# Performance work log

Hardware: AMD Instinct MI355X
Metric: run time of the kernel (lower is better)

The kernel has to match this reference:

```python
import jax, jax.numpy as jnp
import numpy as np

B, D, C = 32, 30, 4        # batch, input spatial, in-channels
KS = 3                     # kernel size per dim
OD = D - KS + 1            # 28 (valid padding, stride 1)
P = OD ** 3                # 21952 output positions
K = (KS ** 3) * C          # 108 taps per output position
F = 4                      # output filters


def _patches(x):
    # x: [B, D, D, D, C] -> [B, P, K]
    xt = jnp.transpose(x, (0, 4, 1, 2, 3))  # NCDHW
    p = jax.lax.conv_general_dilated_patches(
        xt, filter_shape=(KS, KS, KS), window_strides=(1, 1, 1), padding='VALID')
    # p: [B, C*KS^3, OD, OD, OD]
    p = jnp.transpose(p, (0, 2, 3, 4, 1))
    return p.reshape(p.shape[0], P, K)


def _local_conv(x, W):
    # Locally-connected 3D conv (unshared weights) == structured sparse matmul.
    # W: [P, K, F] one weight per (output position, tap, filter).
    return jnp.einsum('bpk,pkf->bpf', _patches(x), W)


def setup_inputs() -> dict:
    key = jax.random.key(0)
    ks = jax.random.split(key, 7)
    x = jax.random.normal(ks[0], (B, D, D, D, C), jnp.float32)
    kernel_loc = jax.random.normal(ks[1], (P, K, F), jnp.float32) * 0.05
    kernel_rho = jax.random.normal(ks[2], (P, K, F), jnp.float32) * 0.1 - 5.0  # softplus -> small scale
    bias = jax.random.normal(ks[3], (F,), jnp.float32) * 0.05
    eps = jax.random.normal(ks[4], (P, K, F), jnp.float32)
    sign_in = jax.random.rademacher(ks[5], (B, D, D, D, C), jnp.float32)
    sign_out = jax.random.rademacher(ks[6], (B, P, F), jnp.float32)
    return dict(x=x, kernel_loc=kernel_loc, kernel_rho=kernel_rho, bias=bias,
                eps=eps, sign_in=sign_in, sign_out=sign_out)


def reference(x, kernel_loc, kernel_rho, bias, eps, sign_in, sign_out):
    # Flipout estimator: deterministic mean path + sign-perturbed noise path.
    scale = jax.nn.softplus(kernel_rho)
    out = _local_conv(x, kernel_loc)                                  # [B, P, F]
    out = out + sign_out * _local_conv(x * sign_in, scale * eps)      # flipout perturbation
    out = out + bias                                                  # per-filter bias (channels_last)
    return out.reshape(x.shape[0], OD, OD, OD, F)
```

## Files before the change

kernel.cpp:

```cpp
#include <hip/hip_runtime.h>


constexpr int Bn   = 32;
constexpr int Dn   = 30;
constexpr int Cn   = 4;
constexpr int ODn  = 28;
constexpr int Pn   = ODn * ODn * ODn;
constexpr int Tt   = 27;
constexpr int Kn   = Tt * Cn;
constexpr int PPB  = 16;
constexpr int THREADS = 256;
constexpr int WSTRIDE = Kn + 1;

__device__ __forceinline__ unsigned bf16rne(float f) {
    unsigned u = __float_as_uint(f);
    return (u + 0x7fffu + ((u >> 16) & 1u)) >> 16;
}
__device__ __forceinline__ float bflo(unsigned u) { return __uint_as_float(u << 16); }
__device__ __forceinline__ float bfhi(unsigned u) { return __uint_as_float(u & 0xffff0000u); }

__global__ __launch_bounds__(THREADS) void lc3d_flipout_kernel(
    const float* __restrict__ x,
    const float* __restrict__ loc,
    const float* __restrict__ rho,
    const float* __restrict__ bias,
    const float* __restrict__ eps,
    const float* __restrict__ sgn_in,
    const float* __restrict__ sgn_out,
    float* __restrict__ out)
{
    __shared__ uint4 w[PPB * WSTRIDE];

    const int tid    = threadIdx.x;
    const int p_base = blockIdx.x * PPB;

    const float4* loc4 = (const float4*)loc + (size_t)p_base * Kn;
    const float4* rho4 = (const float4*)rho + (size_t)p_base * Kn;
    const float4* eps4 = (const float4*)eps + (size_t)p_base * Kn;

    for (int g = tid; g < PPB * Kn; g += THREADS) {
        const int pl = g / Kn;
        const int k  = g - pl * Kn;
        const float4 L = loc4[g];
        const float4 R = rho4[g];
        const float4 E = eps4[g];
        float nx = (R.x > 15.f ? R.x : __logf(1.f + __expf(R.x))) * E.x;
        float ny = (R.y > 15.f ? R.y : __logf(1.f + __expf(R.y))) * E.y;
        float nz = (R.z > 15.f ? R.z : __logf(1.f + __expf(R.z))) * E.z;
        float nw = (R.w > 15.f ? R.w : __logf(1.f + __expf(R.w))) * E.w;
        uint4 pk;
        pk.x = bf16rne(L.x) | (bf16rne(L.y) << 16);
        pk.y = bf16rne(L.z) | (bf16rne(L.w) << 16);
        pk.z = bf16rne(nx)  | (bf16rne(ny) << 16);
        pk.w = bf16rne(nz)  | (bf16rne(nw) << 16);
        w[pl * WSTRIDE + k] = pk;
    }
    __syncthreads();

    const int pl = tid & 15;
    const int bh = tid >> 4;
    const int b0 = bh, b1 = bh + 16;
    const int p  = p_base + pl;
    const int od   = p / (ODn * ODn);
    const int prem = p - od * (ODn * ODn);
    const int oh   = prem / ODn;
    const int ow   = prem - oh * ODn;

    const float4* x4 = (const float4*)x;
    const float4* s4 = (const float4*)sgn_in;
    const size_t v0 = (((size_t)b0 * Dn + od) * Dn + oh) * Dn + ow;
    const size_t v1 = (((size_t)b1 * Dn + od) * Dn + oh) * Dn + ow;
    const uint4* wp = w + pl * WSTRIDE;

    float a00=0.f,a01=0.f,a02=0.f,a03=0.f;
    float a10=0.f,a11=0.f,a12=0.f,a13=0.f;
    float n00=0.f,n01=0.f,n02=0.f,n03=0.f;
    float n10=0.f,n11=0.f,n12=0.f,n13=0.f;

#define CHAN(c, xa_c, sa_c, xb_c, sb_c)                                      \
    {                                                                        \
        const uint4 wv = wp[(c) * Tt + t];                                   \
        const float m0 = bflo(wv.x), m1 = bfhi(wv.x);                        \
        const float m2 = bflo(wv.y), m3 = bfhi(wv.y);                        \
        const float q0 = bflo(wv.z), q1 = bfhi(wv.z);                        \
        const float q2 = bflo(wv.w), q3 = bfhi(wv.w);                        \
        a00 = fmaf(xa_c, m0, a00); a01 = fmaf(xa_c, m1, a01);                \
        a02 = fmaf(xa_c, m2, a02); a03 = fmaf(xa_c, m3, a03);                \
        a10 = fmaf(xb_c, m0, a10); a11 = fmaf(xb_c, m1, a11);                \
        a12 = fmaf(xb_c, m2, a12); a13 = fmaf(xb_c, m3, a13);                \
        const float ya = (xa_c) * (sa_c);                                    \
        const float yb = (xb_c) * (sb_c);                                    \
        n00 = fmaf(ya, q0, n00); n01 = fmaf(ya, q1, n01);                    \
        n02 = fmaf(ya, q2, n02); n03 = fmaf(ya, q3, n03);                    \
        n10 = fmaf(yb, q0, n10); n11 = fmaf(yb, q1, n11);                    \
        n12 = fmaf(yb, q2, n12); n13 = fmaf(yb, q3, n13);                    \
    }

    #pragma unroll
    for (int kd = 0; kd < 3; ++kd) {
        #pragma unroll
        for (int kh = 0; kh < 3; ++kh) {
            const int roff = (kd * Dn + kh) * Dn;
            const float4* xr0 = x4 + v0 + roff;
            const float4* sr0 = s4 + v0 + roff;
            const float4* xr1 = x4 + v1 + roff;
            const float4* sr1 = s4 + v1 + roff;
            #pragma unroll
            for (int kw = 0; kw < 3; ++kw) {
                const int t = (kd * 3 + kh) * 3 + kw;
                const float4 xa = xr0[kw];
                const float4 sa = sr0[kw];
                const float4 xb = xr1[kw];
                const float4 sb = sr1[kw];
                CHAN(0, xa.x, sa.x, xb.x, sb.x);
                CHAN(1, xa.y, sa.y, xb.y, sb.y);
                CHAN(2, xa.z, sa.z, xb.z, sb.z);
                CHAN(3, xa.w, sa.w, xb.w, sb.w);
            }
        }
    }
#undef CHAN

    const float4 bi = *(const float4*)bias;
    const size_t ob0 = (size_t)b0 * Pn + p;
    const size_t ob1 = (size_t)b1 * Pn + p;
    const float4 so0 = ((const float4*)sgn_out)[ob0];
    const float4 so1 = ((const float4*)sgn_out)[ob1];
    float4 o0, o1;
    o0.x = fmaf(so0.x, n00, a00) + bi.x;
    o0.y = fmaf(so0.y, n01, a01) + bi.y;
    o0.z = fmaf(so0.z, n02, a02) + bi.z;
    o0.w = fmaf(so0.w, n03, a03) + bi.w;
    o1.x = fmaf(so1.x, n10, a10) + bi.x;
    o1.y = fmaf(so1.y, n11, a11) + bi.y;
    o1.z = fmaf(so1.z, n12, a12) + bi.z;
    o1.w = fmaf(so1.w, n13, a13) + bi.w;
    ((float4*)out)[ob0] = o0;
    ((float4*)out)[ob1] = o1;
}

extern "C" void kernel_launch(void* const* d_in, const int* in_sizes, int n_in,
                              void* d_out, int out_size, void* d_ws, size_t ws_size,
                              hipStream_t stream) {
    const float* x    = (const float*)d_in[0];
    const float* loc  = (const float*)d_in[1];
    const float* rho  = (const float*)d_in[2];
    const float* bias = (const float*)d_in[3];
    const float* eps  = (const float*)d_in[4];
    const float* si   = (const float*)d_in[5];
    const float* so   = (const float*)d_in[6];
    float* out = (float*)d_out;

    lc3d_flipout_kernel<<<dim3(Pn / PPB), dim3(THREADS), 0, stream>>>(
        x, loc, rho, bias, eps, si, so, out);
}
```

Measured before the change: 217.5 us.

## Use single-wave blocks with XCD-aware tile swizzle and drop barrier

```diff
diff --git a/kernel.cpp b/kernel.cpp
--- a/kernel.cpp
+++ b/kernel.cpp
@@ -8,8 +8,9 @@
 constexpr int Pn   = ODn * ODn * ODn;
 constexpr int Tt   = 27;
 constexpr int Kn   = Tt * Cn;
-constexpr int PPB  = 16;
-constexpr int THREADS = 256;
+constexpr int PPB  = 4;
+constexpr int NT   = Pn / PPB;
+constexpr int THREADS = 64;
 constexpr int WSTRIDE = Kn + 1;
 
 __device__ __forceinline__ unsigned bf16rne(float f) {
@@ -29,18 +30,19 @@
     const float* __restrict__ sgn_out,
     float* __restrict__ out)
 {
-    __shared__ uint4 w[PPB * WSTRIDE];
+    __shared__ uint4 wsh[PPB * WSTRIDE];
 
-    const int tid    = threadIdx.x;
-    const int p_base = blockIdx.x * PPB;
+    const int lane = threadIdx.x;
+
+    const int tile   = (blockIdx.x & 7) * (NT / 8) + (blockIdx.x >> 3);
+    const int p_base = tile * PPB;
 
     const float4* loc4 = (const float4*)loc + (size_t)p_base * Kn;
     const float4* rho4 = (const float4*)rho + (size_t)p_base * Kn;
     const float4* eps4 = (const float4*)eps + (size_t)p_base * Kn;
-
-    for (int g = tid; g < PPB * Kn; g += THREADS) {
-        const int pl = g / Kn;
-        const int k  = g - pl * Kn;
+    for (int g = lane; g < PPB * Kn; g += THREADS) {
+        const int plc = g / Kn;
+        const int k   = g - plc * Kn;
         const float4 L = loc4[g];
         const float4 R = rho4[g];
         const float4 E = eps4[g];
@@ -53,29 +55,25 @@
         pk.y = bf16rne(L.z) | (bf16rne(L.w) << 16);
         pk.z = bf16rne(nx)  | (bf16rne(ny) << 16);
         pk.w = bf16rne(nz)  | (bf16rne(nw) << 16);
-        w[pl * WSTRIDE + k] = pk;
+        wsh[plc * WSTRIDE + k] = pk;
     }
-    __syncthreads();
 
-    const int pl = tid & 15;
-    const int bh = tid >> 4;
+    const int pl = lane & 3;
+    const int bh = lane >> 2;
     const int b0 = bh, b1 = bh + 16;
     const int p  = p_base + pl;
-    const int od   = p / (ODn * ODn);
+    const int od = p / (ODn * ODn);
     const int prem = p - od * (ODn * ODn);
-    const int oh   = prem / ODn;
-    const int ow   = prem - oh * ODn;
-
+    const int oh = prem / ODn;
+    const int ow = prem - oh * ODn;
     const float4* x4 = (const float4*)x;
     const float4* s4 = (const float4*)sgn_in;
     const size_t v0 = (((size_t)b0 * Dn + od) * Dn + oh) * Dn + ow;
     const size_t v1 = (((size_t)b1 * Dn + od) * Dn + oh) * Dn + ow;
-    const uint4* wp = w + pl * WSTRIDE;
+    const uint4* wp = wsh + pl * WSTRIDE;
 
-    float a00=0.f,a01=0.f,a02=0.f,a03=0.f;
-    float a10=0.f,a11=0.f,a12=0.f,a13=0.f;
-    float n00=0.f,n01=0.f,n02=0.f,n03=0.f;
-    float n10=0.f,n11=0.f,n12=0.f,n13=0.f;
+    float a00=0.f,a01=0.f,a02=0.f,a03=0.f, a10=0.f,a11=0.f,a12=0.f,a13=0.f;
+    float n00=0.f,n01=0.f,n02=0.f,n03=0.f, n10=0.f,n11=0.f,n12=0.f,n13=0.f;
 
 #define CHAN(c, xa_c, sa_c, xb_c, sb_c)                                      \
     {                                                                        \
@@ -101,17 +99,13 @@
         #pragma unroll
         for (int kh = 0; kh < 3; ++kh) {
             const int roff = (kd * Dn + kh) * Dn;
-            const float4* xr0 = x4 + v0 + roff;
-            const float4* sr0 = s4 + v0 + roff;
-            const float4* xr1 = x4 + v1 + roff;
-            const float4* sr1 = s4 + v1 + roff;
             #pragma unroll
             for (int kw = 0; kw < 3; ++kw) {
                 const int t = (kd * 3 + kh) * 3 + kw;
-                const float4 xa = xr0[kw];
-                const float4 sa = sr0[kw];
-                const float4 xb = xr1[kw];
-                const float4 sb = sr1[kw];
+                const float4 xa = x4[v0 + roff + kw];
+                const float4 sa = s4[v0 + roff + kw];
+                const float4 xb = x4[v1 + roff + kw];
+                const float4 sb = s4[v1 + roff + kw];
                 CHAN(0, xa.x, sa.x, xb.x, sb.x);
                 CHAN(1, xa.y, sa.y, xb.y, sb.y);
                 CHAN(2, xa.z, sa.z, xb.z, sb.z);
@@ -151,6 +145,6 @@
     const float* so   = (const float*)d_in[6];
     float* out = (float*)d_out;
 
-    lc3d_flipout_kernel<<<dim3(Pn / PPB), dim3(THREADS), 0, stream>>>(
+    lc3d_flipout_kernel<<<dim3(NT), dim3(THREADS), 0, stream>>>(
         x, loc, rho, bias, eps, si, so, out);
 }
```

After: 220.8 us. Within noise of the previous version (+1.5%).
